# Kernel optimization log

Measured on AMD Instinct MI355X. Metric: run time of the kernel, lower is better.

## Reference

```python
import jax, jax.numpy as jnp
import numpy as np

N_NODES = 32000   # total nodes
NUM_GRAPHS = 32   # B
NODES_PER_GRAPH = 1000
N_EDGES = 256000
IN_DIM = 1024
HIDDEN = 256
C = 8             # clusters per graph


def sage_conv(x, src, dst, W_l, b_l, W_r, num_nodes):
    """PyG SAGEConv (mean aggr): out = lin_l(mean_{j in N(i)} x_j) + lin_r(x_i).
    lin_l has bias, lin_r does not. Zero in-degree -> zero aggregation."""
    msg = x[src]  # [E, F] gather from source nodes
    summed = jax.ops.segment_sum(msg, dst, num_segments=num_nodes)          # [N, F]
    cnt = jax.ops.segment_sum(jnp.ones(src.shape, x.dtype), dst, num_segments=num_nodes)  # [N]
    agg = jnp.where(cnt[:, None] > 0, summed / jnp.maximum(cnt, 1.0)[:, None], 0.0)
    return agg @ W_l + b_l + x @ W_r


def setup_inputs() -> dict:
    key = jax.random.key(0)
    ks = jax.random.split(key, 20)
    x = jax.random.normal(ks[0], (N_NODES, IN_DIM), dtype=jnp.float32)
    # edges strictly within each graph (nodes per graph contiguous)
    ge = jax.random.randint(ks[1], (N_EDGES,), 0, NUM_GRAPHS)
    sl = jax.random.randint(ks[2], (N_EDGES,), 0, NODES_PER_GRAPH)
    dl = jax.random.randint(ks[3], (N_EDGES,), 0, NODES_PER_GRAPH)
    edge_index = jnp.stack([ge * NODES_PER_GRAPH + sl, ge * NODES_PER_GRAPH + dl], axis=0)
    batch = jnp.arange(N_NODES, dtype=jnp.int32) // NODES_PER_GRAPH

    def lin(k, fi, fo):
        return jax.random.normal(k, (fi, fo), dtype=jnp.float32) / np.sqrt(fi)

    return {
        "x": x, "edge_index": edge_index, "batch": batch,
        # gnn_embed: SAGEConv(in_dim, hidden)
        "Wl1": lin(ks[4], IN_DIM, HIDDEN), "bl1": jnp.zeros((HIDDEN,), jnp.float32), "Wr1": lin(ks[5], IN_DIM, HIDDEN),
        # gnn_assign: SAGEConv(in_dim, C)
        "Wla": lin(ks[6], IN_DIM, C), "bla": jnp.zeros((C,), jnp.float32), "Wra": lin(ks[7], IN_DIM, C),
        # gnn_embed2: SAGEConv(hidden, hidden)
        "Wl2": lin(ks[8], HIDDEN, HIDDEN), "bl2": jnp.zeros((HIDDEN,), jnp.float32), "Wr2": lin(ks[9], HIDDEN, HIDDEN),
        # classifier MLP
        "Wc1": lin(ks[10], HIDDEN * C, HIDDEN), "bc1": jnp.zeros((HIDDEN,), jnp.float32),
        "Wc2": lin(ks[11], HIDDEN, 1), "bc2": jnp.zeros((1,), jnp.float32),
    }


def reference(x, edge_index, batch, Wl1, bl1, Wr1, Wla, bla, Wra, Wl2, bl2, Wr2, Wc1, bc1, Wc2, bc2):
    src, dst = edge_index[0], edge_index[1]
    n = x.shape[0]
    Z = jax.nn.relu(sage_conv(x, src, dst, Wl1, bl1, Wr1, n))   # [N, H]
    S = sage_conv(x, src, dst, Wla, bla, Wra, n)                 # [N, C]
    Ss = jax.nn.softmax(S, axis=-1)                              # row-softmax assignment
    # Per-graph DiffPool, batched via segment sums (replaces the python loop):
    # X_pool[g] = S_g^T Z_g
    Xp = jax.ops.segment_sum(Ss[:, :, None] * Z[:, None, :], batch, num_segments=NUM_GRAPHS)  # [B,C,H]
    # A_pool[g] = S_g^T A_g S_g  (A binary from to_dense_adj of within-graph edges)
    eg = batch[src]  # graph id per edge
    Ap = jax.ops.segment_sum(Ss[src][:, :, None] * Ss[dst][:, None, :], eg, num_segments=NUM_GRAPHS)  # [B,C,C]
    # dense_to_sparse(block_diag(A_pool)) drops edge weights -> binary block-diag adjacency.
    mask = (Ap != 0).astype(Z.dtype)   # edge i->j where A_pool[g,i,j] != 0
    deg = mask.sum(axis=1)             # in-degree of pooled node j: [B,C]
    agg = jnp.einsum('gij,gih->gjh', mask, Xp)  # mean over source pooled nodes
    agg = jnp.where(deg[:, :, None] > 0, agg / jnp.maximum(deg, 1.0)[:, :, None], 0.0)
    Zp = jax.nn.relu(agg @ Wl2 + bl2 + Xp @ Wr2)  # [B,C,H]
    g = Zp.reshape(NUM_GRAPHS, C * HIDDEN)
    h = jax.nn.relu(g @ Wc1 + bc1)
    return (h @ Wc2 + bc2).squeeze(-1)            # [B]
```

## Files before the change

kernel.cpp:

```cpp
#include <hip/hip_runtime.h>
#include <hip/hip_bf16.h>
#include <math.h>

#define N_NODES 32000
#define NUM_GRAPHS 32
#define NPG 1000
#define N_EDGES 256000
#define IN_DIM 1024
#define HID 256
#define NW 528
#define KBH 1040
#define WS_KS 16896
#define ZWORDS 139776

typedef _Float16 half8 __attribute__((ext_vector_type(8)));
typedef _Float16 half4 __attribute__((ext_vector_type(4)));
typedef float f32x4 __attribute__((ext_vector_type(4)));

__device__ __forceinline__ void gload16(const void* g, void* l) {
  __builtin_amdgcn_global_load_lds((const __attribute__((address_space(1))) void*)g,
                                   (__attribute__((address_space(3))) void*)l, 16, 0, 0);
}

__global__ __launch_bounds__(256) void prep_kernel(
    const float* __restrict__ Wl1, const float* __restrict__ Wr1,
    const float* __restrict__ Wla, const float* __restrict__ Wra,
    _Float16* __restrict__ WsT2, unsigned* __restrict__ zbuf)
{
  const int t = threadIdx.x;
  const int flat = blockIdx.y * 3 + blockIdx.x;
  for (int i = flat * 256 + t; i < ZWORDS; i += 384 * 256) zbuf[i] = 0u;

  const int kslot = blockIdx.y;
  const int n = blockIdx.x * 256 + t;
  if (n >= NW) return;
  const int k0 = kslot * 8;
  half8 o;
#pragma unroll
  for (int i = 0; i < 8; ++i) {
    const int k = k0 + i;
    float v;
    if (n < 256)      v = Wl1[(size_t)k * 256 + n];
    else if (n < 512) v = Wr1[(size_t)k * 256 + n - 256];
    else if (n < 520) v = Wla[(size_t)k * 8 + n - 512];
    else              v = Wra[(size_t)k * 8 + n - 520];
    o[i] = (_Float16)v;
  }
  const int K = kslot >> 2, kb = kslot & 3;
  size_t off;
  if (n < 512) off = (size_t)K * WS_KS + (size_t)(n >> 7) * 4096 + kb * 1024 + (n & 127) * 8;
  else         off = (size_t)K * WS_KS + 16384 + (kb * 128) + (n - 512) * 8;
  *(half8*)&WsT2[off] = o;
}

__global__ __launch_bounds__(256) void xhalf_deg(
    const float* __restrict__ x, _Float16* __restrict__ XH,
    const int* __restrict__ dst, int* __restrict__ deg)
{
  const int e = blockIdx.x * 256 + threadIdx.x;
  if (e < N_EDGES) atomicAdd(&deg[dst[e]], 1);

  const size_t i = ((size_t)blockIdx.x * 256 + threadIdx.x) * 8;
  float4 a = *(const float4*)(x + i);
  float4 b = *(const float4*)(x + i + 4);
  half8 h;
  h[0] = (_Float16)a.x; h[1] = (_Float16)a.y; h[2] = (_Float16)a.z; h[3] = (_Float16)a.w;
  h[4] = (_Float16)b.x; h[5] = (_Float16)b.y; h[6] = (_Float16)b.z; h[7] = (_Float16)b.w;
  *(half8*)&XH[i] = h;
}

__global__ __launch_bounds__(256) void gemm_mfma(
    const _Float16* __restrict__ XH, const _Float16* __restrict__ WsT2,
    _Float16* __restrict__ C)
{
  const int orig = blockIdx.x;
  const int xcd = orig & 7, idx = orig >> 3;
  const int g = (xcd < 2 ? xcd * 157 : 314 + (xcd - 2) * 156) + idx;
  const int pm = g / 5, nb = g % 5;
  const int m0 = pm * 128;

  __shared__ _Float16 AH[4 * KBH];
  __shared__ _Float16 Bs[4 * KBH];

  const int tid = threadIdx.x;
  const int w = tid >> 6, l = tid & 63;
  const int wr = w >> 1, wc = w & 1;
  const int r16 = l & 15, kb4 = l >> 4;

  int lpA[2];
  const _Float16* gA[2];
  const _Float16* gB[2];
#pragma unroll
  for (int j = 0; j < 2; ++j) {
    const int c = tid + j * 256;
    const int kb = c >> 7, row = c & 127;
    lpA[j] = kb * KBH + row * 8;
    gA[j] = XH + (size_t)(m0 + row) * IN_DIM + kb * 8;
    gB[j] = WsT2 + nb * 4096 + (size_t)c * 8;
  }

  if (nb < 4) {
    f32x4 acc[4][4] = {};
    for (int ks = 0; ks < 32; ++ks) {
      const size_t ko = (size_t)ks * 32;
      const size_t bo = (size_t)ks * WS_KS;
      __syncthreads();
      gload16(gA[0] + ko, &AH[lpA[0]]);
      gload16(gA[1] + ko, &AH[lpA[1]]);
      gload16(gB[0] + bo, &Bs[lpA[0]]);
      gload16(gB[1] + bo, &Bs[lpA[1]]);
      __syncthreads();

      half8 bf[4];
#pragma unroll
      for (int n = 0; n < 4; ++n)
        bf[n] = *(half8*)&Bs[kb4 * KBH + (wc * 64 + n * 16 + r16) * 8];
#pragma unroll
      for (int m = 0; m < 4; ++m) {
        half8 ah = *(half8*)&AH[kb4 * KBH + (wr * 64 + m * 16 + r16) * 8];
#pragma unroll
        for (int n = 0; n < 4; ++n)
          acc[m][n] = __builtin_amdgcn_mfma_f32_16x16x32_f16(ah, bf[n], acc[m][n], 0, 0, 0);
      }
    }

    const int crow0 = m0 + wr * 64 + ((l >> 4) << 2);
    const int ccol0 = nb * 128 + wc * 64 + r16;
#pragma unroll
    for (int m = 0; m < 4; ++m)
#pragma unroll
      for (int n = 0; n < 4; ++n)
#pragma unroll
        for (int r = 0; r < 4; ++r)
          C[(size_t)(crow0 + m * 16 + r) * NW + ccol0 + n * 16] = (_Float16)acc[m][n][r];
  } else {
    f32x4 acc2[2] = {};
    for (int ks = 0; ks < 32; ++ks) {
      const size_t ko = (size_t)ks * 32;
      const size_t bo = (size_t)ks * WS_KS + 16384;
      __syncthreads();
      gload16(gA[0] + ko, &AH[lpA[0]]);
      gload16(gA[1] + ko, &AH[lpA[1]]);
      if (tid < 64) gload16(WsT2 + bo + tid * 8, &Bs[tid * 8]);
      __syncthreads();

      half8 bf = *(half8*)&Bs[(kb4 * 16 + r16) * 8];
#pragma unroll
      for (int m = 0; m < 2; ++m) {
        half8 ah = *(half8*)&AH[kb4 * KBH + (w * 32 + m * 16 + r16) * 8];
        acc2[m] = __builtin_amdgcn_mfma_f32_16x16x32_f16(ah, bf, acc2[m], 0, 0, 0);
      }
    }
    const int crow0 = m0 + w * 32 + ((l >> 4) << 2);
    const int ccol0 = 512 + r16;
#pragma unroll
    for (int m = 0; m < 2; ++m)
#pragma unroll
      for (int r = 0; r < 4; ++r)
        C[(size_t)(crow0 + m * 16 + r) * NW + ccol0] = (_Float16)acc2[m][r];
  }
}

__global__ __launch_bounds__(1024) void scan_kernel(const int* __restrict__ deg,
                                                    int* __restrict__ offsets) {
  __shared__ int part[1024];
  const int t = threadIdx.x;
  const int base = t * 32;
  int vals[32];
  if (t < 1000) {
#pragma unroll
    for (int j = 0; j < 8; ++j) {
      int4 v = *(const int4*)(deg + base + j * 4);
      vals[j * 4 + 0] = v.x; vals[j * 4 + 1] = v.y;
      vals[j * 4 + 2] = v.z; vals[j * 4 + 3] = v.w;
    }
  } else {
#pragma unroll
    for (int i = 0; i < 32; ++i) vals[i] = 0;
  }
  int local[32];
  int s = 0;
#pragma unroll
  for (int i = 0; i < 32; ++i) { local[i] = s; s += vals[i]; }
  part[t] = s;
  __syncthreads();
  for (int off = 1; off < 1024; off <<= 1) {
    int v = (t >= off) ? part[t - off] : 0;
    __syncthreads();
    part[t] += v;
    __syncthreads();
  }
  int excl = part[t] - s;
  if (t < 1000) {
#pragma unroll
    for (int i = 0; i < 32; ++i) offsets[base + i] = excl + local[i];
  }
  if (t == 1023) offsets[N_NODES] = part[1023];
}

__global__ void scatter_kernel(const int* __restrict__ src, const int* __restrict__ dst,
                               const int* __restrict__ offsets, int* __restrict__ cursor,
                               int* __restrict__ srcSorted) {
  int e = blockIdx.x * blockDim.x + threadIdx.x;
  if (e < N_EDGES) {
    int d = dst[e];
    int pos = offsets[d] + atomicAdd(&cursor[d], 1);
    srcSorted[pos] = src[e];
  }
}

__global__ __launch_bounds__(256) void aggregate_node(
    const _Float16* __restrict__ C,
    const int* __restrict__ offsets, const int* __restrict__ srcSorted,
    const float* __restrict__ bl1, const float* __restrict__ bla,
    _Float16* __restrict__ Zh, float* __restrict__ Ss)
{
  const int bid = blockIdx.x;
  const int wv = threadIdx.x >> 6, lane = threadIdx.x & 63;
  const int node = (bid & 7) * 4000 + (bid >> 3) * 4 + wv;
  const int b = offsets[node], e = offsets[node + 1];
  const int cnt = e - b;
  const float4 blv = *(const float4*)(bl1 + 4 * lane);
  float a0 = 0.f, a1 = 0.f, a2 = 0.f, a3 = 0.f, sp = 0.f;
  int p = b;
  int sNext = (p < e) ? srcSorted[p] : 0;
  while (p < e) {
    const int s = sNext;
    ++p;
    sNext = (p < e) ? srcSorted[p] : 0;
    const _Float16* row = C + (size_t)s * NW;
    half4 v = *(const half4*)(row + 4 * lane);
    float spv = 0.f;
    if (lane < 8) spv = (float)row[512 + lane];
    a0 += (float)v[0]; a1 += (float)v[1]; a2 += (float)v[2]; a3 += (float)v[3];
    sp += spv;
  }
  const float inv = (cnt > 0) ? 1.f / (float)cnt : 0.f;
  const _Float16* self = C + (size_t)node * NW;
  half4 sv = *(const half4*)(self + 256 + 4 * lane);
  half4 zo;
  zo[0] = (_Float16)fmaxf(a0 * inv + blv.x + (float)sv[0], 0.f);
  zo[1] = (_Float16)fmaxf(a1 * inv + blv.y + (float)sv[1], 0.f);
  zo[2] = (_Float16)fmaxf(a2 * inv + blv.z + (float)sv[2], 0.f);
  zo[3] = (_Float16)fmaxf(a3 * inv + blv.w + (float)sv[3], 0.f);
  *(half4*)(Zh + (size_t)node * 256 + 4 * lane) = zo;

  float sval = 0.f;
  if (lane < 8) sval = sp * inv + bla[lane] + (float)self[520 + lane];
  float m = sval;
  m = fmaxf(m, __shfl_xor(m, 1));
  m = fmaxf(m, __shfl_xor(m, 2));
  m = fmaxf(m, __shfl_xor(m, 4));
  float ex = expf(sval - m);
  float su = ex;
  su += __shfl_xor(su, 1);
  su += __shfl_xor(su, 2);
  su += __shfl_xor(su, 4);
  if (lane < 8) Ss[(size_t)node * 8 + lane] = ex / su;
}

__global__ __launch_bounds__(256) void pool_kernel(
    const float* __restrict__ Ss, const _Float16* __restrict__ Zh,
    const int* __restrict__ offsets, const int* __restrict__ srcSorted,
    float* __restrict__ Xp, float* __restrict__ Ap)
{
  const int g = blockIdx.x >> 3;
  const int chunk = blockIdx.x & 7;
  const int n0 = g * NPG + chunk * 125;
  const int t = threadIdx.x;
  __shared__ float lSs[125][8];
  __shared__ float lAg[125][8];
  __shared__ float apTmp[4][64];

  if (t < 125) {
    const int node = n0 + t;
    float4 s0 = *(const float4*)&Ss[(size_t)node * 8];
    float4 s1 = *(const float4*)&Ss[(size_t)node * 8 + 4];
    lSs[t][0] = s0.x; lSs[t][1] = s0.y; lSs[t][2] = s0.z; lSs[t][3] = s0.w;
    lSs[t][4] = s1.x; lSs[t][5] = s1.y; lSs[t][6] = s1.z; lSs[t][7] = s1.w;
    float a[8] = {0.f, 0.f, 0.f, 0.f, 0.f, 0.f, 0.f, 0.f};
    const int b = offsets[node], e = offsets[node + 1];
    for (int p = b; p < e; ++p) {
      const int s = srcSorted[p];
      float4 v0 = *(const float4*)&Ss[(size_t)s * 8];
      float4 v1 = *(const float4*)&Ss[(size_t)s * 8 + 4];
      a[0] += v0.x; a[1] += v0.y; a[2] += v0.z; a[3] += v0.w;
      a[4] += v1.x; a[5] += v1.y; a[6] += v1.z; a[7] += v1.w;
    }
#pragma unroll
    for (int c = 0; c < 8; ++c) lAg[t][c] = a[c];
  }
  __syncthreads();
  {
    const int sl = t >> 6, i = (t >> 3) & 7, j = t & 7;
    float acc = 0.f;
    for (int n = sl; n < 125; n += 4) acc += lAg[n][i] * lSs[n][j];
    apTmp[sl][((i << 3) | j)] = acc;
  }
  __syncthreads();
  if (t < 64) atomicAdd(&Ap[g * 64 + t], apTmp[0][t] + apTmp[1][t] + apTmp[2][t] + apTmp[3][t]);
  float xc[8] = {0.f, 0.f, 0.f, 0.f, 0.f, 0.f, 0.f, 0.f};
  for (int n = 0; n < 125; ++n) {
    float zv = (float)Zh[(size_t)(n0 + n) * 256 + t];
#pragma unroll
    for (int c = 0; c < 8; ++c) xc[c] = fmaf(lSs[n][c], zv, xc[c]);
  }
#pragma unroll
  for (int c = 0; c < 8; ++c)
    atomicAdd(&Xp[((size_t)g * 8 + c) * 256 + t], xc[c]);
}

__global__ __launch_bounds__(256) void zpcls_kernel(
    const float* __restrict__ Xp, const float* __restrict__ Ap,
    const float* __restrict__ Wl2, const float* __restrict__ bl2,
    const float* __restrict__ Wr2, const float* __restrict__ Wc1,
    float* __restrict__ Hacc)
{
  const int g = blockIdx.x >> 3;
  const int j = blockIdx.x & 7;
  const int c = threadIdx.x;
  __shared__ float lXp[8][256];
  __shared__ float agg[256];
  __shared__ float zrow[256];
  __shared__ float lAp[64];
#pragma unroll
  for (int i = 0; i < 8; ++i) lXp[i][c] = Xp[((size_t)g * 8 + i) * 256 + c];
  if (c < 64) lAp[c] = Ap[g * 64 + c];
  __syncthreads();
  {
    float d = 0.f, s = 0.f;
#pragma unroll
    for (int i = 0; i < 8; ++i) {
      bool m = (lAp[i * 8 + j] != 0.f);
      d += m ? 1.f : 0.f;
      s += m ? lXp[i][c] : 0.f;
    }
    agg[c] = (d > 0.f) ? s / fmaxf(d, 1.f) : 0.f;
  }
  __syncthreads();
  float az = bl2[c];
#pragma unroll 8
  for (int k = 0; k < 256; ++k)
    az += agg[k] * Wl2[(size_t)k * 256 + c] + lXp[j][k] * Wr2[(size_t)k * 256 + c];
  zrow[c] = fmaxf(az, 0.f);
  __syncthreads();
  float h = 0.f;
  const float* wc1 = Wc1 + (size_t)(j * 256) * 256 + c;
#pragma unroll 8
  for (int k = 0; k < 256; ++k)
    h = fmaf(zrow[k], wc1[(size_t)k * 256], h);
  atomicAdd(&Hacc[g * 256 + c], h);
}

__global__ __launch_bounds__(256) void out_kernel(
    const float* __restrict__ Hacc, const float* __restrict__ bc1,
    const float* __restrict__ Wc2, const float* __restrict__ bc2,
    float* __restrict__ out)
{
  const int g = blockIdx.x;
  const int t = threadIdx.x;
  __shared__ float red[256];
  red[t] = fmaxf(Hacc[g * 256 + t] + bc1[t], 0.f) * Wc2[t];
  __syncthreads();
  for (int off = 128; off > 0; off >>= 1) {
    if (t < off) red[t] += red[t + off];
    __syncthreads();
  }
  if (t == 0) out[g] = red[0] + bc2[0];
}

extern "C" void kernel_launch(void* const* d_in, const int* in_sizes, int n_in,
                              void* d_out, int out_size, void* d_ws, size_t ws_size,
                              hipStream_t stream) {
  const float* x   = (const float*)d_in[0];
  const int*   ei  = (const int*)d_in[1];
  const float* Wl1 = (const float*)d_in[3];
  const float* bl1 = (const float*)d_in[4];
  const float* Wr1 = (const float*)d_in[5];
  const float* Wla = (const float*)d_in[6];
  const float* bla = (const float*)d_in[7];
  const float* Wra = (const float*)d_in[8];
  const float* Wl2 = (const float*)d_in[9];
  const float* bl2 = (const float*)d_in[10];
  const float* Wr2 = (const float*)d_in[11];
  const float* Wc1 = (const float*)d_in[12];
  const float* bc1 = (const float*)d_in[13];
  const float* Wc2 = (const float*)d_in[14];
  const float* bc2 = (const float*)d_in[15];
  float* out = (float*)d_out;

  _Float16* C    = (_Float16*)d_ws;
  _Float16* WsT2 = C + (size_t)32000 * NW;
  _Float16* XH   = WsT2 + 540672;
  _Float16* Zh   = XH + (size_t)32000 * 1024;
  float* Ss   = (float*)(Zh + (size_t)32000 * 256);
  float* Xp   = Ss + 256000;
  float* Ap   = Xp + 65536;
  int* deg     = (int*)(Ap + 2048);
  int* cursor  = deg + 32000;
  float* Hacc  = (float*)(cursor + 32000);
  int* offsets = (int*)(Hacc + 8192);
  int* srcS    = offsets + 32001;
  unsigned* zbuf = (unsigned*)Xp;

  const int* src = ei;
  const int* dst = ei + N_EDGES;

  prep_kernel<<<dim3(3, 128), 256, 0, stream>>>(Wl1, Wr1, Wla, Wra, WsT2, zbuf);
  xhalf_deg<<<16000, 256, 0, stream>>>(x, XH, dst, deg);
  gemm_mfma<<<1250, 256, 0, stream>>>(XH, WsT2, C);
  scan_kernel<<<1, 1024, 0, stream>>>(deg, offsets);
  scatter_kernel<<<1000, 256, 0, stream>>>(src, dst, offsets, cursor, srcS);
  aggregate_node<<<8000, 256, 0, stream>>>(C, offsets, srcS, bl1, bla, Zh, Ss);
  pool_kernel<<<256, 256, 0, stream>>>(Ss, Zh, offsets, srcS, Xp, Ap);
  zpcls_kernel<<<256, 256, 0, stream>>>(Xp, Ap, Wl2, bl2, Wr2, Wc1, Hacc);
  out_kernel<<<32, 256, 0, stream>>>(Hacc, bc1, Wc2, bc2, out);
}
```

Baseline: 208.9 us.

## Fuse fp32-to-fp16 conversion of x into the GEMM A-tile load

```diff
diff --git a/kernel.cpp b/kernel.cpp
--- a/kernel.cpp
+++ b/kernel.cpp
@@ -10,6 +10,7 @@
 #define HID 256
 #define NW 528
 #define KBH 1040
+#define AFB 1032
 #define WS_KS 16896
 #define ZWORDS 139776
 
@@ -53,24 +54,13 @@
   *(half8*)&WsT2[off] = o;
 }
 
-__global__ __launch_bounds__(256) void xhalf_deg(
-    const float* __restrict__ x, _Float16* __restrict__ XH,
-    const int* __restrict__ dst, int* __restrict__ deg)
-{
-  const int e = blockIdx.x * 256 + threadIdx.x;
+__global__ void count_deg(const int* __restrict__ dst, int* __restrict__ deg) {
+  int e = blockIdx.x * blockDim.x + threadIdx.x;
   if (e < N_EDGES) atomicAdd(&deg[dst[e]], 1);
-
-  const size_t i = ((size_t)blockIdx.x * 256 + threadIdx.x) * 8;
-  float4 a = *(const float4*)(x + i);
-  float4 b = *(const float4*)(x + i + 4);
-  half8 h;
-  h[0] = (_Float16)a.x; h[1] = (_Float16)a.y; h[2] = (_Float16)a.z; h[3] = (_Float16)a.w;
-  h[4] = (_Float16)b.x; h[5] = (_Float16)b.y; h[6] = (_Float16)b.z; h[7] = (_Float16)b.w;
-  *(half8*)&XH[i] = h;
 }
 
 __global__ __launch_bounds__(256) void gemm_mfma(
-    const _Float16* __restrict__ XH, const _Float16* __restrict__ WsT2,
+    const float* __restrict__ x, const _Float16* __restrict__ WsT2,
     _Float16* __restrict__ C)
 {
   const int orig = blockIdx.x;
@@ -79,7 +69,7 @@
   const int pm = g / 5, nb = g % 5;
   const int m0 = pm * 128;
 
-  __shared__ _Float16 AH[4 * KBH];
+  __shared__ float    AF[4 * AFB];
   __shared__ _Float16 Bs[4 * KBH];
 
   const int tid = threadIdx.x;
@@ -87,15 +77,22 @@
   const int wr = w >> 1, wc = w & 1;
   const int r16 = l & 15, kb4 = l >> 4;
 
-  int lpA[2];
-  const _Float16* gA[2];
+  int lpAf[4];
+  const float* gA[4];
+#pragma unroll
+  for (int j = 0; j < 4; ++j) {
+    const int c = tid + j * 256;
+    const int koct = c >> 8, rem = c & 255;
+    lpAf[j] = koct * AFB + rem * 4;
+    gA[j] = x + (size_t)(m0 + (rem >> 1)) * IN_DIM + koct * 8 + (rem & 1) * 4;
+  }
+  int lpB[2];
   const _Float16* gB[2];
 #pragma unroll
   for (int j = 0; j < 2; ++j) {
     const int c = tid + j * 256;
-    const int kb = c >> 7, row = c & 127;
-    lpA[j] = kb * KBH + row * 8;
-    gA[j] = XH + (size_t)(m0 + row) * IN_DIM + kb * 8;
+    const int kb = c >> 7, col = c & 127;
+    lpB[j] = kb * KBH + col * 8;
     gB[j] = WsT2 + nb * 4096 + (size_t)c * 8;
   }
 
@@ -105,10 +102,10 @@
       const size_t ko = (size_t)ks * 32;
       const size_t bo = (size_t)ks * WS_KS;
       __syncthreads();
-      gload16(gA[0] + ko, &AH[lpA[0]]);
-      gload16(gA[1] + ko, &AH[lpA[1]]);
-      gload16(gB[0] + bo, &Bs[lpA[0]]);
-      gload16(gB[1] + bo, &Bs[lpA[1]]);
+#pragma unroll
+      for (int j = 0; j < 4; ++j) gload16(gA[j] + ko, &AF[lpAf[j]]);
+      gload16(gB[0] + bo, &Bs[lpB[0]]);
+      gload16(gB[1] + bo, &Bs[lpB[1]]);
       __syncthreads();
 
       half8 bf[4];
@@ -117,7 +114,13 @@
         bf[n] = *(half8*)&Bs[kb4 * KBH + (wc * 64 + n * 16 + r16) * 8];
 #pragma unroll
       for (int m = 0; m < 4; ++m) {
-        half8 ah = *(half8*)&AH[kb4 * KBH + (wr * 64 + m * 16 + r16) * 8];
+        const float* ap = &AF[kb4 * AFB + (wr * 64 + m * 16 + r16) * 8];
+        float fa[8];
+        *(f32x4*)&fa[0] = *(const f32x4*)ap;
+        *(f32x4*)&fa[4] = *(const f32x4*)(ap + 4);
+        half8 ah;
+#pragma unroll
+        for (int i = 0; i < 8; ++i) ah[i] = (_Float16)fa[i];
 #pragma unroll
         for (int n = 0; n < 4; ++n)
           acc[m][n] = __builtin_amdgcn_mfma_f32_16x16x32_f16(ah, bf[n], acc[m][n], 0, 0, 0);
@@ -139,16 +142,22 @@
       const size_t ko = (size_t)ks * 32;
       const size_t bo = (size_t)ks * WS_KS + 16384;
       __syncthreads();
-      gload16(gA[0] + ko, &AH[lpA[0]]);
-      gload16(gA[1] + ko, &AH[lpA[1]]);
+#pragma unroll
+      for (int j = 0; j < 4; ++j) gload16(gA[j] + ko, &AF[lpAf[j]]);
       if (tid < 64) gload16(WsT2 + bo + tid * 8, &Bs[tid * 8]);
       __syncthreads();
 
-      half8 bf = *(half8*)&Bs[(kb4 * 16 + r16) * 8];
+      half8 bfs = *(half8*)&Bs[(kb4 * 16 + r16) * 8];
 #pragma unroll
       for (int m = 0; m < 2; ++m) {
-        half8 ah = *(half8*)&AH[kb4 * KBH + (w * 32 + m * 16 + r16) * 8];
-        acc2[m] = __builtin_amdgcn_mfma_f32_16x16x32_f16(ah, bf, acc2[m], 0, 0, 0);
+        const float* ap = &AF[kb4 * AFB + (w * 32 + m * 16 + r16) * 8];
+        float fa[8];
+        *(f32x4*)&fa[0] = *(const f32x4*)ap;
+        *(f32x4*)&fa[4] = *(const f32x4*)(ap + 4);
+        half8 ah;
+#pragma unroll
+        for (int i = 0; i < 8; ++i) ah[i] = (_Float16)fa[i];
+        acc2[m] = __builtin_amdgcn_mfma_f32_16x16x32_f16(ah, bfs, acc2[m], 0, 0, 0);
       }
     }
     const int crow0 = m0 + w * 32 + ((l >> 4) << 2);
@@ -391,8 +400,7 @@
 
   _Float16* C    = (_Float16*)d_ws;
   _Float16* WsT2 = C + (size_t)32000 * NW;
-  _Float16* XH   = WsT2 + 540672;
-  _Float16* Zh   = XH + (size_t)32000 * 1024;
+  _Float16* Zh   = WsT2 + 540672;
   float* Ss   = (float*)(Zh + (size_t)32000 * 256);
   float* Xp   = Ss + 256000;
   float* Ap   = Xp + 65536;
@@ -407,8 +415,8 @@
   const int* dst = ei + N_EDGES;
 
   prep_kernel<<<dim3(3, 128), 256, 0, stream>>>(Wl1, Wr1, Wla, Wra, WsT2, zbuf);
-  xhalf_deg<<<16000, 256, 0, stream>>>(x, XH, dst, deg);
-  gemm_mfma<<<1250, 256, 0, stream>>>(XH, WsT2, C);
+  count_deg<<<1000, 256, 0, stream>>>(dst, deg);
+  gemm_mfma<<<1250, 256, 0, stream>>>(x, WsT2, C);
   scan_kernel<<<1, 1024, 0, stream>>>(deg, offsets);
   scatter_kernel<<<1000, 256, 0, stream>>>(src, dst, offsets, cursor, srcS);
   aggregate_node<<<8000, 256, 0, stream>>>(C, offsets, srcS, bl1, bla, Zh, Ss);
```

Result: faster. 198.2 us (-5.1%).

## Merge weight prep, fp16 cast and degree count; fold scan into GEMM grid

Applied to the files above, without the earlier changes.

```diff
diff --git a/kernel.cpp b/kernel.cpp
--- a/kernel.cpp
+++ b/kernel.cpp
@@ -11,7 +11,7 @@
 #define NW 528
 #define KBH 1040
 #define WS_KS 16896
-#define ZWORDS 139776
+#define ZWORDS 75776
 
 typedef _Float16 half8 __attribute__((ext_vector_type(8)));
 typedef _Float16 half4 __attribute__((ext_vector_type(4)));
@@ -22,17 +22,38 @@
                                    (__attribute__((address_space(3))) void*)l, 16, 0, 0);
 }
 
-__global__ __launch_bounds__(256) void prep_kernel(
+__global__ __launch_bounds__(256) void prep_all(
     const float* __restrict__ Wl1, const float* __restrict__ Wr1,
     const float* __restrict__ Wla, const float* __restrict__ Wra,
-    _Float16* __restrict__ WsT2, unsigned* __restrict__ zbuf)
-{
+    const float* __restrict__ x, _Float16* __restrict__ WsT2,
+    _Float16* __restrict__ XH, unsigned* __restrict__ zbuf,
+    const int* __restrict__ dst, int* __restrict__ deg)
+{
+  const int bid = blockIdx.x;
   const int t = threadIdx.x;
-  const int flat = blockIdx.y * 3 + blockIdx.x;
-  for (int i = flat * 256 + t; i < ZWORDS; i += 384 * 256) zbuf[i] = 0u;
-
-  const int kslot = blockIdx.y;
-  const int n = blockIdx.x * 256 + t;
+  if (bid < 512) {
+    for (int i = bid * 256 + t; i < ZWORDS; i += 512 * 256) zbuf[i] = 0u;
+  }
+
+  if (bid < 16000) {
+    const size_t i = ((size_t)bid * 256 + t) * 8;
+    float4 a = *(const float4*)(x + i);
+    float4 b = *(const float4*)(x + i + 4);
+    half8 h;
+    h[0] = (_Float16)a.x; h[1] = (_Float16)a.y; h[2] = (_Float16)a.z; h[3] = (_Float16)a.w;
+    h[4] = (_Float16)b.x; h[5] = (_Float16)b.y; h[6] = (_Float16)b.z; h[7] = (_Float16)b.w;
+    *(half8*)&XH[i] = h;
+    return;
+  }
+  if (bid >= 16384) {
+    const int e0 = (bid - 16384) * 2000;
+    for (int i = t; i < 2000; i += 256) atomicAdd(&deg[dst[e0 + i]], 1);
+    return;
+  }
+
+  const int fb = bid - 16000;
+  const int kslot = fb / 3;
+  const int n = (fb % 3) * 256 + t;
   if (n >= NW) return;
   const int k0 = kslot * 8;
   half8 o;
@@ -53,36 +74,43 @@
   *(half8*)&WsT2[off] = o;
 }
 
-__global__ __launch_bounds__(256) void xhalf_deg(
-    const float* __restrict__ x, _Float16* __restrict__ XH,
-    const int* __restrict__ dst, int* __restrict__ deg)
-{
-  const int e = blockIdx.x * 256 + threadIdx.x;
-  if (e < N_EDGES) atomicAdd(&deg[dst[e]], 1);
-
-  const size_t i = ((size_t)blockIdx.x * 256 + threadIdx.x) * 8;
-  float4 a = *(const float4*)(x + i);
-  float4 b = *(const float4*)(x + i + 4);
-  half8 h;
-  h[0] = (_Float16)a.x; h[1] = (_Float16)a.y; h[2] = (_Float16)a.z; h[3] = (_Float16)a.w;
-  h[4] = (_Float16)b.x; h[5] = (_Float16)b.y; h[6] = (_Float16)b.z; h[7] = (_Float16)b.w;
-  *(half8*)&XH[i] = h;
-}
-
 __global__ __launch_bounds__(256) void gemm_mfma(
     const _Float16* __restrict__ XH, const _Float16* __restrict__ WsT2,
-    _Float16* __restrict__ C)
-{
+    _Float16* __restrict__ C, const int* __restrict__ deg, int* __restrict__ offsets)
+{
+  __shared__ _Float16 AH[4 * KBH];
+  __shared__ _Float16 Bs[4 * KBH];
+
   const int orig = blockIdx.x;
+  const int tid = threadIdx.x;
+
+  if (orig == 1250) {
+    int* part = (int*)AH;
+    const int base = tid * 125;
+    int s = 0;
+    for (int i = 0; i < 125; ++i) s += deg[base + i];
+    part[tid] = s;
+    __syncthreads();
+    for (int off = 1; off < 256; off <<= 1) {
+      int v = (tid >= off) ? part[tid - off] : 0;
+      __syncthreads();
+      part[tid] += v;
+      __syncthreads();
+    }
+    int run = part[tid] - s;
+    for (int i = 0; i < 125; ++i) {
+      offsets[base + i] = run;
+      run += deg[base + i];
+    }
+    if (tid == 255) offsets[N_NODES] = part[255];
+    return;
+  }
+
   const int xcd = orig & 7, idx = orig >> 3;
   const int g = (xcd < 2 ? xcd * 157 : 314 + (xcd - 2) * 156) + idx;
   const int pm = g / 5, nb = g % 5;
   const int m0 = pm * 128;
 
-  __shared__ _Float16 AH[4 * KBH];
-  __shared__ _Float16 Bs[4 * KBH];
-
-  const int tid = threadIdx.x;
   const int w = tid >> 6, l = tid & 63;
   const int wr = w >> 1, wc = w & 1;
   const int r16 = l & 15, kb4 = l >> 4;
@@ -159,43 +187,6 @@
       for (int r = 0; r < 4; ++r)
         C[(size_t)(crow0 + m * 16 + r) * NW + ccol0] = (_Float16)acc2[m][r];
   }
-}
-
-__global__ __launch_bounds__(1024) void scan_kernel(const int* __restrict__ deg,
-                                                    int* __restrict__ offsets) {
-  __shared__ int part[1024];
-  const int t = threadIdx.x;
-  const int base = t * 32;
-  int vals[32];
-  if (t < 1000) {
-#pragma unroll
-    for (int j = 0; j < 8; ++j) {
-      int4 v = *(const int4*)(deg + base + j * 4);
-      vals[j * 4 + 0] = v.x; vals[j * 4 + 1] = v.y;
-      vals[j * 4 + 2] = v.z; vals[j * 4 + 3] = v.w;
-    }
-  } else {
-#pragma unroll
-    for (int i = 0; i < 32; ++i) vals[i] = 0;
-  }
-  int local[32];
-  int s = 0;
-#pragma unroll
-  for (int i = 0; i < 32; ++i) { local[i] = s; s += vals[i]; }
-  part[t] = s;
-  __syncthreads();
-  for (int off = 1; off < 1024; off <<= 1) {
-    int v = (t >= off) ? part[t - off] : 0;
-    __syncthreads();
-    part[t] += v;
-    __syncthreads();
-  }
-  int excl = part[t] - s;
-  if (t < 1000) {
-#pragma unroll
-    for (int i = 0; i < 32; ++i) offsets[base + i] = excl + local[i];
-  }
-  if (t == 1023) offsets[N_NODES] = part[1023];
 }
 
 __global__ void scatter_kernel(const int* __restrict__ src, const int* __restrict__ dst,
@@ -396,20 +387,19 @@
   float* Ss   = (float*)(Zh + (size_t)32000 * 256);
   float* Xp   = Ss + 256000;
   float* Ap   = Xp + 65536;
-  int* deg     = (int*)(Ap + 2048);
+  float* Hacc = Ap + 2048;
+  int* deg     = (int*)(Hacc + 8192);
   int* cursor  = deg + 32000;
-  float* Hacc  = (float*)(cursor + 32000);
-  int* offsets = (int*)(Hacc + 8192);
+  int* offsets = cursor + 32000;
   int* srcS    = offsets + 32001;
   unsigned* zbuf = (unsigned*)Xp;
 
   const int* src = ei;
   const int* dst = ei + N_EDGES;
 
-  prep_kernel<<<dim3(3, 128), 256, 0, stream>>>(Wl1, Wr1, Wla, Wra, WsT2, zbuf);
-  xhalf_deg<<<16000, 256, 0, stream>>>(x, XH, dst, deg);
-  gemm_mfma<<<1250, 256, 0, stream>>>(XH, WsT2, C);
-  scan_kernel<<<1, 1024, 0, stream>>>(deg, offsets);
+  hipMemsetAsync(deg, 0, 64000 * sizeof(int), stream);
+  prep_all<<<16512, 256, 0, stream>>>(Wl1, Wr1, Wla, Wra, x, WsT2, XH, zbuf, dst, deg);
+  gemm_mfma<<<1251, 256, 0, stream>>>(XH, WsT2, C, deg, offsets);
   scatter_kernel<<<1000, 256, 0, stream>>>(src, dst, offsets, cursor, srcS);
   aggregate_node<<<8000, 256, 0, stream>>>(C, offsets, srcS, bl1, bla, Zh, Ss);
   pool_kernel<<<256, 256, 0, stream>>>(Ss, Zh, offsets, srcS, Xp, Ap);
```

Measured after the change: 206.7 us. About the same (-1.0%).
